# Optimization experiments

Measured on AMD Instinct MI355X. Metric: run time of the kernel, lower is better.

The kernel has to match this reference:

```python
import jax, jax.numpy as jnp
import numpy as np

N_NODES = 50000


def gcn_conv(x, W, b, src, dst, num_nodes):
    # GCNConv (PyG defaults): h = D^{-1/2} (A + I) D^{-1/2} x W + b
    h = x @ W  # [N, out_dim]
    deg = jax.ops.segment_sum(jnp.ones(src.shape[0], h.dtype), dst, num_segments=num_nodes)
    dinv = jnp.where(deg > 0, jax.lax.rsqrt(deg), 0.0)
    norm = dinv[src] * dinv[dst]  # [E]
    out = jax.ops.segment_sum(h[src] * norm[:, None], dst, num_segments=num_nodes)
    return out + b


def setup_inputs() -> dict:
    key = jax.random.key(0)
    k1, k2, k3, k4 = jax.random.split(key, 4)
    x = jax.random.normal(k1, (N_NODES, 512), dtype=jnp.float32)
    ei = jax.random.randint(k2, (2, 800000), 0, N_NODES, dtype=jnp.int64)
    # Glorot-like init for GCN linear weights; PyG bias init zeros
    W1 = jax.random.normal(k3, (512, 128), dtype=jnp.float32) * (1.0 / np.sqrt(512))
    b1 = jnp.zeros((128,), dtype=jnp.float32)
    W2 = jax.random.normal(k4, (128, 64), dtype=jnp.float32) * (1.0 / np.sqrt(128))
    b2 = jnp.zeros((64,), dtype=jnp.float32)
    return {"x": x, "ei": ei, "W1": W1, "b1": b1, "W2": W2, "b2": b2}


def reference(x, ei, W1, b1, W2, b2):
    n = x.shape[0]
    loops = jnp.arange(n, dtype=ei.dtype)
    src = jnp.concatenate([ei[0], loops])  # add self-loops (PyG default)
    dst = jnp.concatenate([ei[1], loops])
    h = jax.nn.relu(gcn_conv(x, W1, b1, src, dst, n))
    return jax.nn.relu(gcn_conv(h, W2, b2, src, dst, n))
```

## Files before the change

### kernel.cpp

```cpp
#include <hip/hip_runtime.h>


#define N_FEAT0 512
#define N_FEAT1 128
#define N_FEAT2 64
#define SLACK 64

typedef _Float16 f16x8 __attribute__((ext_vector_type(8)));
typedef float f32x16 __attribute__((ext_vector_type(16)));


__global__ void k_prep(const float* __restrict__ W1, const float* __restrict__ W2,
                       _Float16* __restrict__ Wt, _Float16* __restrict__ Wt2,
                       int* __restrict__ cnt, int n) {
    int idx = blockIdx.x * 256 + threadIdx.x;
    if (idx < 65536) {
        int k = idx >> 7;
        int c = idx & 127;
        Wt[(size_t)c * 512 + k] = (_Float16)W1[idx];
    } else if (idx < 65536 + 8192) {
        int j = idx - 65536;
        int k = j >> 6;
        int c = j & 63;
        Wt2[(size_t)c * 128 + k] = (_Float16)W2[j];
    }
    if (idx < n) cnt[idx] = 0;
}


__global__ __launch_bounds__(256) void k_fused(const float* __restrict__ X,
                                               const _Float16* __restrict__ Wt,
                                               const int* __restrict__ src,
                                               const int* __restrict__ dst,
                                               int* __restrict__ cnt,
                                               int* __restrict__ srcs_pad,
                                               _Float16* __restrict__ H,
                                               int n, int E, int G2) {
    __shared__ __align__(16) _Float16 ah[4][32][8];
    __shared__ __align__(16) _Float16 wh[4][128][8];
    const int tid = threadIdx.x;

    if ((int)blockIdx.x < G2) {
        const int t = blockIdx.x * 256 + tid;
        const int base = t * 4;
        if (base + 3 < E) {
            int4 d = *(const int4*)(dst + base);
            int4 s = *(const int4*)(src + base);
            int p0 = atomicAdd(&cnt[d.x], 1);
            int p1 = atomicAdd(&cnt[d.y], 1);
            int p2 = atomicAdd(&cnt[d.z], 1);
            int p3 = atomicAdd(&cnt[d.w], 1);
            if (p0 < SLACK) srcs_pad[(size_t)d.x * SLACK + p0] = s.x;
            if (p1 < SLACK) srcs_pad[(size_t)d.y * SLACK + p1] = s.y;
            if (p2 < SLACK) srcs_pad[(size_t)d.z * SLACK + p2] = s.z;
            if (p3 < SLACK) srcs_pad[(size_t)d.w * SLACK + p3] = s.w;
        } else {
            for (int i = base; i < E; i++) {
                int d = dst[i];
                int p = atomicAdd(&cnt[d], 1);
                if (p < SLACK) srcs_pad[(size_t)d * SLACK + p] = src[i];
            }
        }
        return;
    }

    const int bid = blockIdx.x - G2;
    const int lane = tid & 63;
    const int w = tid >> 6;
    const int row0 = bid * 32;

    f32x16 acc0 = {};

    const int arow = tid >> 2;
    const int aoct = tid & 3;
    const bool ax = (tid < 128);
    const int gr = row0 + arow;
    const float* xrow = X + (size_t)gr * N_FEAT0 + aoct * 8;

    const int c0 = tid >> 2,          o0 = tid & 3;
    const int c1 = (tid + 256) >> 2,  o1 = tid & 3;
    const _Float16* wp0 = Wt + (size_t)c0 * 512 + o0 * 8;
    const _Float16* wp1 = Wt + (size_t)c1 * 512 + o1 * 8;

    float4 xa0, xb0, xa1, xb1;
    {
        const float4 z = make_float4(0.f, 0.f, 0.f, 0.f);
        if (ax && gr < n) {
            xa0 = ((const float4*)xrow)[0];
            xb0 = ((const float4*)xrow)[1];
            xa1 = ((const float4*)(xrow + 32))[0];
            xb1 = ((const float4*)(xrow + 32))[1];
        } else {
            xa0 = z; xb0 = z; xa1 = z; xb1 = z;
        }
    }
    f16x8 w0r = *(const f16x8*)wp0;
    f16x8 w1r = *(const f16x8*)wp1;

#define GCN_STEP(PA, PB, K0)                                                 \
    {                                                                        \
        if (ax) {                                                            \
            f16x8 hv;                                                        \
            hv[0] = (_Float16)PA.x; hv[1] = (_Float16)PA.y;                  \
            hv[2] = (_Float16)PA.z; hv[3] = (_Float16)PA.w;                  \
            hv[4] = (_Float16)PB.x; hv[5] = (_Float16)PB.y;                  \
            hv[6] = (_Float16)PB.z; hv[7] = (_Float16)PB.w;                  \
            *(f16x8*)(&ah[aoct][arow][0]) = hv;                              \
        }                                                                    \
        *(f16x8*)(&wh[o0][c0][0]) = w0r;                                     \
        *(f16x8*)(&wh[o1][c1][0]) = w1r;                                     \
        const int kx = (K0) + 64;                                            \
        if (kx < N_FEAT0 && ax && gr < n) {                                  \
            PA = ((const float4*)(xrow + kx))[0];                            \
            PB = ((const float4*)(xrow + kx))[1];                            \
        }                                                                    \
        const int kw = (K0) + 32;                                            \
        if (kw < N_FEAT0) {                                                  \
            w0r = *(const f16x8*)(wp0 + kw);                                 \
            w1r = *(const f16x8*)(wp1 + kw);                                 \
        }                                                                    \
        __syncthreads();                                                     \
        _Pragma("unroll")                                                    \
        for (int kb = 0; kb < 2; kb++) {                                     \
            const int oct = kb * 2 + (lane >> 5);                            \
            f16x8 a = *(const f16x8*)(&ah[oct][(lane & 31)][0]);             \
            f16x8 b = *(const f16x8*)(&wh[oct][w * 32 + (lane & 31)][0]);    \
            acc0 = __builtin_amdgcn_mfma_f32_32x32x16_f16(a, b, acc0, 0, 0, 0); \
        }                                                                    \
        __syncthreads();                                                     \
    }

    for (int t2 = 0; t2 < 8; t2++) {
        GCN_STEP(xa0, xb0, t2 * 64)
        GCN_STEP(xa1, xb1, t2 * 64 + 32)
    }
#undef GCN_STEP

    const int col = w * 32 + (lane & 31);
#pragma unroll
    for (int rq = 0; rq < 4; rq++)
#pragma unroll
        for (int rr = 0; rr < 4; rr++) {
            const int reg = rq * 4 + rr;
            const int row = row0 + rr + 8 * rq + 4 * (lane >> 5);
            if (row < n)
                H[(size_t)row * N_FEAT1 + col] = (_Float16)acc0[reg];
        }
}

__global__ __launch_bounds__(256) void k_gemm2_mfma(const _Float16* __restrict__ A,
                                                    const _Float16* __restrict__ Wt2,
                                                    const int* __restrict__ cnt,
                                                    _Float16* __restrict__ H2, int n) {
    __shared__ __align__(16) _Float16 ah[16][128][8];
    __shared__ __align__(16) _Float16 bh[16][64][8];
    const int tid = threadIdx.x;
    const int lane = tid & 63;
    const int w = tid >> 6;
    const int row0 = blockIdx.x * 128;

#pragma unroll
    for (int it = 0; it < 8; it++) {
        int u = tid + it * 256;
        int r = u >> 4;
        int o = u & 15;
        int gr = row0 + r;
        f16x8 v = {};
        if (gr < n) v = *(const f16x8*)(A + (size_t)gr * 128 + o * 8);
        *(f16x8*)(&ah[o][r][0]) = v;
    }
#pragma unroll
    for (int it = 0; it < 4; it++) {
        int u = tid + it * 256;
        int c = u >> 4;
        int o = u & 15;
        *(f16x8*)(&bh[o][c][0]) = *(const f16x8*)(Wt2 + (size_t)c * 128 + o * 8);
    }
    __syncthreads();

    f32x16 acc0 = {}, acc1 = {};
#pragma unroll
    for (int s = 0; s < 8; s++) {
        const int oct = s * 2 + (lane >> 5);
        f16x8 a  = *(const f16x8*)(&ah[oct][w * 32 + (lane & 31)][0]);
        f16x8 b0 = *(const f16x8*)(&bh[oct][(lane & 31)][0]);
        f16x8 b1 = *(const f16x8*)(&bh[oct][32 + (lane & 31)][0]);
        acc0 = __builtin_amdgcn_mfma_f32_32x32x16_f16(a, b0, acc0, 0, 0, 0);
        acc1 = __builtin_amdgcn_mfma_f32_32x32x16_f16(a, b1, acc1, 0, 0, 0);
    }

#pragma unroll
    for (int rq = 0; rq < 4; rq++)
#pragma unroll
        for (int rr = 0; rr < 4; rr++) {
            const int row = row0 + w * 32 + rr + 8 * rq + 4 * (lane >> 5);
            if (row < n) {
                const float di = rsqrtf((float)(cnt[row] + 1));
                const int reg = rq * 4 + rr;
                H2[(size_t)row * N_FEAT2 + (lane & 31)] = (_Float16)(acc0[reg] * di);
                H2[(size_t)row * N_FEAT2 + 32 + (lane & 31)] = (_Float16)(acc1[reg] * di);
            }
        }
}

__global__ __launch_bounds__(256) void k_gather128(const int* __restrict__ srcs_pad,
                                                   const int* __restrict__ cnt,
                                                   const _Float16* __restrict__ H,
                                                   const float* __restrict__ bias,
                                                   _Float16* __restrict__ out, int n) {
    const int node = blockIdx.x * 16 + (threadIdx.x >> 4);
    const int li = threadIdx.x & 15;
    if (node >= n) return;
    const f16x8* __restrict__ H8 = (const f16x8*)H;
    f16x8 sv = H8[(size_t)node * 16 + li];
    const int c = cnt[node];
    const float di = rsqrtf((float)(c + 1));
    float a[8];
#pragma unroll
    for (int q = 0; q < 8; q++) a[q] = di * (float)sv[q];
    const int e = c < SLACK ? c : SLACK;
    const int* __restrict__ sp = srcs_pad + (size_t)node * SLACK;
    int j = 0;
    for (; j + 3 < e; j += 4) {
        int s0 = sp[j], s1 = sp[j + 1], s2 = sp[j + 2], s3 = sp[j + 3];
        float d0 = rsqrtf((float)(cnt[s0] + 1));
        float d1 = rsqrtf((float)(cnt[s1] + 1));
        float d2 = rsqrtf((float)(cnt[s2] + 1));
        float d3 = rsqrtf((float)(cnt[s3] + 1));
        f16x8 v0 = H8[(size_t)s0 * 16 + li];
        f16x8 v1 = H8[(size_t)s1 * 16 + li];
        f16x8 v2 = H8[(size_t)s2 * 16 + li];
        f16x8 v3 = H8[(size_t)s3 * 16 + li];
#pragma unroll
        for (int q = 0; q < 8; q++)
            a[q] += (d0 * (float)v0[q] + d1 * (float)v1[q]) +
                    (d2 * (float)v2[q] + d3 * (float)v3[q]);
    }
    for (; j < e; j++) {
        int s0 = sp[j];
        float d0 = rsqrtf((float)(cnt[s0] + 1));
        f16x8 v0 = H8[(size_t)s0 * 16 + li];
#pragma unroll
        for (int q = 0; q < 8; q++) a[q] += d0 * (float)v0[q];
    }
    float4 b0 = *(const float4*)(bias + li * 8);
    float4 b1 = *(const float4*)(bias + li * 8 + 4);
    f16x8 r;
    r[0] = (_Float16)fmaxf(a[0] * di + b0.x, 0.f);
    r[1] = (_Float16)fmaxf(a[1] * di + b0.y, 0.f);
    r[2] = (_Float16)fmaxf(a[2] * di + b0.z, 0.f);
    r[3] = (_Float16)fmaxf(a[3] * di + b0.w, 0.f);
    r[4] = (_Float16)fmaxf(a[4] * di + b1.x, 0.f);
    r[5] = (_Float16)fmaxf(a[5] * di + b1.y, 0.f);
    r[6] = (_Float16)fmaxf(a[6] * di + b1.z, 0.f);
    r[7] = (_Float16)fmaxf(a[7] * di + b1.w, 0.f);
    ((f16x8*)out)[(size_t)node * 16 + li] = r;
}

__global__ __launch_bounds__(256) void k_gather64(const int* __restrict__ srcs_pad,
                                                  const int* __restrict__ cnt,
                                                  const _Float16* __restrict__ H,
                                                  const float* __restrict__ bias,
                                                  float* __restrict__ out, int n) {
    const int node = blockIdx.x * 32 + (threadIdx.x >> 3);
    const int li = threadIdx.x & 7;
    if (node >= n) return;
    const f16x8* __restrict__ H8 = (const f16x8*)H;
    f16x8 sv = H8[(size_t)node * 8 + li];
    float a[8];
#pragma unroll
    for (int q = 0; q < 8; q++) a[q] = (float)sv[q];
    const int c = cnt[node];
    const float di = rsqrtf((float)(c + 1));
    const int e = c < SLACK ? c : SLACK;
    const int* __restrict__ sp = srcs_pad + (size_t)node * SLACK;
    int j = 0;
    for (; j + 3 < e; j += 4) {
        int s0 = sp[j], s1 = sp[j + 1], s2 = sp[j + 2], s3 = sp[j + 3];
        f16x8 v0 = H8[(size_t)s0 * 8 + li];
        f16x8 v1 = H8[(size_t)s1 * 8 + li];
        f16x8 v2 = H8[(size_t)s2 * 8 + li];
        f16x8 v3 = H8[(size_t)s3 * 8 + li];
#pragma unroll
        for (int q = 0; q < 8; q++)
            a[q] += ((float)v0[q] + (float)v1[q]) + ((float)v2[q] + (float)v3[q]);
    }
    for (; j < e; j++) {
        f16x8 v0 = H8[(size_t)sp[j] * 8 + li];
#pragma unroll
        for (int q = 0; q < 8; q++) a[q] += (float)v0[q];
    }
    float4 b0 = *(const float4*)(bias + li * 8);
    float4 b1 = *(const float4*)(bias + li * 8 + 4);
    float4 r0, r1;
    r0.x = fmaxf(a[0] * di + b0.x, 0.f);
    r0.y = fmaxf(a[1] * di + b0.y, 0.f);
    r0.z = fmaxf(a[2] * di + b0.z, 0.f);
    r0.w = fmaxf(a[3] * di + b0.w, 0.f);
    r1.x = fmaxf(a[4] * di + b1.x, 0.f);
    r1.y = fmaxf(a[5] * di + b1.y, 0.f);
    r1.z = fmaxf(a[6] * di + b1.z, 0.f);
    r1.w = fmaxf(a[7] * di + b1.w, 0.f);
    float* op = out + (size_t)node * N_FEAT2 + li * 8;
    *(float4*)op = r0;
    *(float4*)(op + 4) = r1;
}


extern "C" void kernel_launch(void* const* d_in, const int* in_sizes, int n_in,
                              void* d_out, int out_size, void* d_ws, size_t ws_size,
                              hipStream_t stream) {
    const float* x  = (const float*)d_in[0];
    const int*   ei = (const int*)d_in[1];
    const float* W1 = (const float*)d_in[2];
    const float* b1 = (const float*)d_in[3];
    const float* W2 = (const float*)d_in[4];
    const float* b2 = (const float*)d_in[5];
    float* out = (float*)d_out;

    const int n = in_sizes[0] / N_FEAT0;
    const int E = in_sizes[1] / 2;
    const int* src = ei;
    const int* dst = ei + E;

    char* p = (char*)d_ws;
    _Float16* h16      = (_Float16*)p;
    _Float16* agg16    = (_Float16*)(p + 12800000);
    _Float16* h2_16    = (_Float16*)(p + 25600000);
    int*      cnt      = (int*)(p + 32000000);
    int*      srcs_pad = (int*)(p + 32200064);
    _Float16* Wt       = (_Float16*)(p + 45000064);
    _Float16* Wt2      = (_Float16*)(p + 45131136);

    const int B = 256;
    const int nprep = (65536 + 8192 > n ? 65536 + 8192 : n);
    const int G2 = ((E + 3) / 4 + B - 1) / B;
    const int G1 = (n + 31) / 32;

    k_prep<<<(nprep + B - 1) / B, B, 0, stream>>>(W1, W2, Wt, Wt2, cnt, n);
    k_fused<<<G2 + G1, B, 0, stream>>>(x, Wt, src, dst, cnt, srcs_pad, h16, n, E, G2);
    k_gather128<<<(n + 15) / 16, B, 0, stream>>>(srcs_pad, cnt, h16, b1, agg16, n);
    k_gemm2_mfma<<<(n + 127) / 128, B, 0, stream>>>(agg16, Wt2, cnt, h2_16, n);
    k_gather64<<<(n + 31) / 32, B, 0, stream>>>(srcs_pad, cnt, h2_16, b2, out, n);
}
```

Before: 155.8 us.

## Split edge scatter from GEMM1 and prescale rows by source degree norm

Separates the fused edge-counting/scatter and layer-1 GEMM kernel into two launches so the GEMM can read the final degree counts. The GEMM epilogue then multiplies each output row by its own inverse-sqrt degree, and the layer-1 gather no longer does a per-neighbor degree lookup and rsqrt. This removes a random cnt read per edge in the gather, at the cost of an extra launch and losing the overlap between the atomic scatter and the GEMM.

New measurement: 146.0 us, median of 2. 1.07x faster.

```diff
diff --git a/kernel.cpp b/kernel.cpp
--- a/kernel.cpp
+++ b/kernel.cpp
@@ -28,46 +28,40 @@
 }
 
 
-__global__ __launch_bounds__(256) void k_fused(const float* __restrict__ X,
-                                               const _Float16* __restrict__ Wt,
-                                               const int* __restrict__ src,
-                                               const int* __restrict__ dst,
-                                               int* __restrict__ cnt,
-                                               int* __restrict__ srcs_pad,
-                                               _Float16* __restrict__ H,
-                                               int n, int E, int G2) {
+__global__ void k_count_scatter(const int* __restrict__ src, const int* __restrict__ dst,
+                                int* __restrict__ cnt, int* __restrict__ srcs_pad, int E) {
+    const int t = blockIdx.x * blockDim.x + threadIdx.x;
+    const int base = t * 4;
+    if (base + 3 < E) {
+        int4 d = *(const int4*)(dst + base);
+        int4 s = *(const int4*)(src + base);
+        int p0 = atomicAdd(&cnt[d.x], 1);
+        int p1 = atomicAdd(&cnt[d.y], 1);
+        int p2 = atomicAdd(&cnt[d.z], 1);
+        int p3 = atomicAdd(&cnt[d.w], 1);
+        if (p0 < SLACK) srcs_pad[(size_t)d.x * SLACK + p0] = s.x;
+        if (p1 < SLACK) srcs_pad[(size_t)d.y * SLACK + p1] = s.y;
+        if (p2 < SLACK) srcs_pad[(size_t)d.z * SLACK + p2] = s.z;
+        if (p3 < SLACK) srcs_pad[(size_t)d.w * SLACK + p3] = s.w;
+    } else {
+        for (int i = base; i < E; i++) {
+            int d = dst[i];
+            int p = atomicAdd(&cnt[d], 1);
+            if (p < SLACK) srcs_pad[(size_t)d * SLACK + p] = src[i];
+        }
+    }
+}
+
+__global__ __launch_bounds__(256) void k_gemm1_mfma(const float* __restrict__ X,
+                                                    const _Float16* __restrict__ Wt,
+                                                    const int* __restrict__ cnt,
+                                                    _Float16* __restrict__ H, int n) {
     __shared__ __align__(16) _Float16 ah[4][32][8];
     __shared__ __align__(16) _Float16 wh[4][128][8];
     const int tid = threadIdx.x;
-
-    if ((int)blockIdx.x < G2) {
-        const int t = blockIdx.x * 256 + tid;
-        const int base = t * 4;
-        if (base + 3 < E) {
-            int4 d = *(const int4*)(dst + base);
-            int4 s = *(const int4*)(src + base);
-            int p0 = atomicAdd(&cnt[d.x], 1);
-            int p1 = atomicAdd(&cnt[d.y], 1);
-            int p2 = atomicAdd(&cnt[d.z], 1);
-            int p3 = atomicAdd(&cnt[d.w], 1);
-            if (p0 < SLACK) srcs_pad[(size_t)d.x * SLACK + p0] = s.x;
-            if (p1 < SLACK) srcs_pad[(size_t)d.y * SLACK + p1] = s.y;
-            if (p2 < SLACK) srcs_pad[(size_t)d.z * SLACK + p2] = s.z;
-            if (p3 < SLACK) srcs_pad[(size_t)d.w * SLACK + p3] = s.w;
-        } else {
-            for (int i = base; i < E; i++) {
-                int d = dst[i];
-                int p = atomicAdd(&cnt[d], 1);
-                if (p < SLACK) srcs_pad[(size_t)d * SLACK + p] = src[i];
-            }
-        }
-        return;
-    }
-
-    const int bid = blockIdx.x - G2;
     const int lane = tid & 63;
     const int w = tid >> 6;
-    const int row0 = bid * 32;
+    const int row0 = blockIdx.x * 32;
 
     f32x16 acc0 = {};
 
@@ -143,8 +137,10 @@
         for (int rr = 0; rr < 4; rr++) {
             const int reg = rq * 4 + rr;
             const int row = row0 + rr + 8 * rq + 4 * (lane >> 5);
-            if (row < n)
-                H[(size_t)row * N_FEAT1 + col] = (_Float16)acc0[reg];
+            if (row < n) {
+                float di = rsqrtf((float)(cnt[row] + 1));
+                H[(size_t)row * N_FEAT1 + col] = (_Float16)(acc0[reg] * di);
+            }
         }
 }
 
@@ -203,6 +199,7 @@
         }
 }
 
+
 __global__ __launch_bounds__(256) void k_gather128(const int* __restrict__ srcs_pad,
                                                    const int* __restrict__ cnt,
                                                    const _Float16* __restrict__ H,
@@ -213,35 +210,28 @@
     if (node >= n) return;
     const f16x8* __restrict__ H8 = (const f16x8*)H;
     f16x8 sv = H8[(size_t)node * 16 + li];
+    float a[8];
+#pragma unroll
+    for (int q = 0; q < 8; q++) a[q] = (float)sv[q];
     const int c = cnt[node];
     const float di = rsqrtf((float)(c + 1));
-    float a[8];
-#pragma unroll
-    for (int q = 0; q < 8; q++) a[q] = di * (float)sv[q];
     const int e = c < SLACK ? c : SLACK;
     const int* __restrict__ sp = srcs_pad + (size_t)node * SLACK;
     int j = 0;
     for (; j + 3 < e; j += 4) {
         int s0 = sp[j], s1 = sp[j + 1], s2 = sp[j + 2], s3 = sp[j + 3];
-        float d0 = rsqrtf((float)(cnt[s0] + 1));
-        float d1 = rsqrtf((float)(cnt[s1] + 1));
-        float d2 = rsqrtf((float)(cnt[s2] + 1));
-        float d3 = rsqrtf((float)(cnt[s3] + 1));
         f16x8 v0 = H8[(size_t)s0 * 16 + li];
         f16x8 v1 = H8[(size_t)s1 * 16 + li];
         f16x8 v2 = H8[(size_t)s2 * 16 + li];
         f16x8 v3 = H8[(size_t)s3 * 16 + li];
 #pragma unroll
         for (int q = 0; q < 8; q++)
-            a[q] += (d0 * (float)v0[q] + d1 * (float)v1[q]) +
-                    (d2 * (float)v2[q] + d3 * (float)v3[q]);
+            a[q] += ((float)v0[q] + (float)v1[q]) + ((float)v2[q] + (float)v3[q]);
     }
     for (; j < e; j++) {
-        int s0 = sp[j];
-        float d0 = rsqrtf((float)(cnt[s0] + 1));
-        f16x8 v0 = H8[(size_t)s0 * 16 + li];
-#pragma unroll
-        for (int q = 0; q < 8; q++) a[q] += d0 * (float)v0[q];
+        f16x8 v0 = H8[(size_t)sp[j] * 16 + li];
+#pragma unroll
+        for (int q = 0; q < 8; q++) a[q] += (float)v0[q];
     }
     float4 b0 = *(const float4*)(bias + li * 8);
     float4 b1 = *(const float4*)(bias + li * 8 + 4);
@@ -334,12 +324,13 @@
 
     const int B = 256;
     const int nprep = (65536 + 8192 > n ? 65536 + 8192 : n);
-    const int G2 = ((E + 3) / 4 + B - 1) / B;
-    const int G1 = (n + 31) / 32;
 
     k_prep<<<(nprep + B - 1) / B, B, 0, stream>>>(W1, W2, Wt, Wt2, cnt, n);
-    k_fused<<<G2 + G1, B, 0, stream>>>(x, Wt, src, dst, cnt, srcs_pad, h16, n, E, G2);
+    k_count_scatter<<<((E + 3) / 4 + B - 1) / B, B, 0, stream>>>(src, dst, cnt, srcs_pad, E);
+
+    k_gemm1_mfma<<<(n + 31) / 32, B, 0, stream>>>(x, Wt, cnt, h16, n);
     k_gather128<<<(n + 15) / 16, B, 0, stream>>>(srcs_pad, cnt, h16, b1, agg16, n);
+
     k_gemm2_mfma<<<(n + 127) / 128, B, 0, stream>>>(agg16, Wt2, cnt, h2_16, n);
     k_gather64<<<(n + 31) / 32, B, 0, stream>>>(srcs_pad, cnt, h2_16, b2, out, n);
 }
```
